# Kernel tuning notes

Hardware: AMD Instinct MI355X
Metric: run time of the kernel (lower is better)

## Reference

```python
import jax, jax.numpy as jnp
import numpy as np

ALPHA = 0.4
MAX_STEPS = 10
GATE_WARMUP = 1.0

def _l2n(x):  # F.normalize(dim=-1), eps=1e-12
    return x / jnp.maximum(jnp.linalg.norm(x, axis=-1, keepdims=True), 1e-12)

def _ln(x, g, b):  # nn.LayerNorm, eps=1e-5
    m = jnp.mean(x, -1, keepdims=True)
    v = jnp.mean((x - m) ** 2, -1, keepdims=True)
    return (x - m) * jax.lax.rsqrt(v + 1e-5) * g + b

def _gelu(x):  # torch F.gelu default = exact erf
    return jax.nn.gelu(x, approximate=False)

def setup_inputs() -> dict:
    key = jax.random.key(0)
    ks = jax.random.split(key, 12)
    B, T, V, D, H = 4, 256, 50257, 768, 3072
    f32 = jnp.float32
    s = lambda k, shape, sc: jax.random.normal(k, shape, dtype=f32) * sc
    return {
        'token_ids': jax.random.randint(ks[0], (B, T), 0, V),
        'embedding': s(ks[1], (V, D), 0.02),      # nn.Embedding table
        'V0': s(ks[2], (D, H), 0.02), 'b0': jnp.zeros((H,), f32),  # hierarchy layer 0
        'V1': s(ks[3], (H, D), 0.02), 'b1': jnp.zeros((D,), f32),  # hierarchy layer 1
        'W1': s(ks[4], (D, D), 0.005), 'c1': jnp.zeros((D,), f32), # core_proj[0]
        'W2': s(ks[5], (D, D), 0.005), 'c2': jnp.zeros((D,), f32), # core_proj[2]
        'Wg': s(ks[6], (2 * D, D), 0.005), 'bg': jnp.zeros((D,), f32),  # gate_proj
        'Wt': s(ks[7], (D, D), 0.01),              # temporal_proj (no bias)
        'gamma': jnp.ones((D,), f32), 'beta': jnp.zeros((D,), f32),    # out_norm
        'Wl': s(ks[8], (D, V), 0.02),              # lm_head (no bias)
        'R_weight': s(ks[9], (D, D), 0.01),        # buffer (orthogonal-ish, small)
    }

def reference(token_ids, embedding, V0, b0, V1, b1, W1, c1, W2, c2, Wg, bg, Wt, gamma, beta, Wl, R_weight):
    B = token_ids.shape[0]
    D = embedding.shape[1]

    def step(carry, idx):
        h_prev, x2 = carry  # h_prev: [B,D] recurrent state; x2: settled hierarchy state [B,D]
        emb = _l2n(embedding[idx])                       # [B,D]
        h_prev_d = jax.lax.stop_gradient(h_prev)         # .detach()
        temporal_raw = h_prev_d @ R_weight               # [B,D]
        ctx = emb + ALPHA * temporal_raw
        # hierarchy.infer_and_learn under no_grad: iterative relaxation toward the
        # feedforward settled state over max_steps iterations.
        ctx_d = jax.lax.stop_gradient(ctx)
        target = _gelu(_gelu(ctx_d @ V0 + b0) @ V1 + b1)
        x2 = jax.lax.fori_loop(0, MAX_STEPS, lambda i, x: 0.5 * x + 0.5 * target, x2)
        x2 = jax.lax.stop_gradient(x2)
        core_settled = _l2n(x2)
        # differentiable shadow path through V0/b0/V1/b1
        core_shadow = _l2n(_gelu(_gelu(ctx @ V0 + b0) @ V1 + b1))
        core_blended = 0.5 * core_shadow + 0.5 * core_settled
        core_feat = _gelu(core_blended @ W1 + c1) @ W2 + c2      # core_proj MLP
        temporal_feat = temporal_raw @ Wt
        gate = jax.nn.sigmoid(jnp.concatenate([emb, core_feat], axis=-1) @ Wg + bg)
        g = gate * GATE_WARMUP
        h_t = g * (core_feat + ALPHA * temporal_feat) + (1.0 - g) * emb
        h_t = _ln(h_t, gamma, beta)
        logits = h_t @ Wl                                # [B,V]
        return (jax.lax.stop_gradient(h_t), x2), logits

    init = (jnp.zeros((B, D), embedding.dtype), jnp.zeros((B, D), embedding.dtype))
    _, logits = jax.lax.scan(step, init, token_ids.T)    # [T,B,V]
    return jnp.transpose(logits, (1, 0, 2))              # [B,T,V]
```

## Files before the change

### kernel.cpp

```cpp
#include <hip/hip_runtime.h>


typedef __attribute__((ext_vector_type(8))) short short8;
typedef __attribute__((ext_vector_type(4))) float f32x4;
typedef unsigned long long u64;

__device__ __forceinline__ unsigned short f2b(float f){
  unsigned int u = __builtin_bit_cast(unsigned int, f);
  u += 0x7fffu + ((u >> 16) & 1u);
  return (unsigned short)(u >> 16);
}
__device__ __forceinline__ float b2f(unsigned short v){
  return __builtin_bit_cast(float, ((unsigned int)v) << 16);
}
__device__ __forceinline__ float geluf(float x){
  return 0.5f * x * (1.0f + erff(x * 0.70710678118654752440f));
}
__device__ __forceinline__ float wsum(float v){
  #pragma unroll
  for (int o = 32; o; o >>= 1) v += __shfl_xor(v, o, 64);
  return v;
}
__device__ __forceinline__ u64 pk3t(float a, float b, float c, unsigned tag){
  return (u64)f2b(a) | ((u64)f2b(b) << 16) | ((u64)f2b(c) << 32) | ((u64)(tag & 0xffffu) << 48);
}
__device__ __forceinline__ void st64(u64* p, u64 v){
  __hip_atomic_store(p, v, __ATOMIC_RELAXED, __HIP_MEMORY_SCOPE_AGENT);
}
__device__ __forceinline__ void stflag(int* p, int v){
  __hip_atomic_store(p, v, __ATOMIC_RELAXED, __HIP_MEMORY_SCOPE_AGENT);
}
__device__ __forceinline__ int ldflag(const int* p){
  return __hip_atomic_load(p, __ATOMIC_RELAXED, __HIP_MEMORY_SCOPE_AGENT);
}
__device__ __forceinline__ void vm0(){ asm volatile("s_waitcnt vmcnt(0)" ::: "memory"); }

#define F0(ph,g) (((ph)*256 + (g))*16)
#define F1(ph,a) (16384 + ((ph)*16 + (a))*16)

__global__ __launch_bounds__(256) void transpose_f2b(
    const float* __restrict__ src, unsigned short* __restrict__ dst,
    int N, int rowoff)
{
  __shared__ unsigned short tile[32][33];
  const int nb = blockIdx.x * 32, kb = blockIdx.y * 32;
  const int tx = threadIdx.x & 31, ty = threadIdx.x >> 5;
  #pragma unroll
  for (int i = 0; i < 4; ++i) {
    int k = kb + ty + 8*i, n = nb + tx;
    unsigned short v = 0;
    if (n < N) v = f2b(src[(size_t)(rowoff + k)*N + n]);
    tile[ty + 8*i][tx] = v;
  }
  __syncthreads();
  #pragma unroll
  for (int i = 0; i < 4; ++i) {
    int n = nb + ty + 8*i;
    if (n < N) dst[(size_t)n*768 + kb + tx] = tile[tx][ty + 8*i];
  }
}

__global__ __launch_bounds__(256) void embed_kernel(
    const int* __restrict__ tok, const float* __restrict__ emb,
    float* __restrict__ emb_all)
{
  const int row = blockIdx.x, tid = threadIdx.x;
  const int id = tok[row];
  const float* e = emb + (size_t)id * 768;
  float v0 = e[tid], v1 = e[tid+256], v2 = e[tid+512];
  float ssq = wsum(v0*v0 + v1*v1 + v2*v2);
  __shared__ float red[4];
  if ((tid & 63) == 0) red[tid >> 6] = ssq;
  __syncthreads();
  float inv = 1.0f / fmaxf(sqrtf(red[0]+red[1]+red[2]+red[3]), 1e-12f);
  float* o = emb_all + (size_t)row * 768;
  o[tid] = v0*inv; o[tid+256] = v1*inv; o[tid+512] = v2*inv;
}

__global__ void gbias_kernel(const float* __restrict__ c2,
                             const float* __restrict__ Wg,
                             float* __restrict__ gbias)
{
  int c = blockIdx.x * 256 + threadIdx.x;
  if (c >= 768) return;
  float s = 0.f;
  for (int k = 0; k < 768; ++k) s += c2[k] * Wg[(size_t)(768 + k)*768 + c];
  gbias[c] = s;
}

template<int BMODE>
__global__ __launch_bounds__(256) void gemm_kernel(
    const float* __restrict__ A, const void* __restrict__ Bp,
    float* __restrict__ C, const float* __restrict__ bias,
    int M, int N, int q, int r)
{
  const int x = blockIdx.x;
  const int s = blockIdx.y;
  const int mtiles = M >> 6;
  const int cnt_x = q + (x < r ? 1 : 0);
  if (s >= cnt_x * mtiles) return;
  const int off_x = x*q + (x < r ? x : r);
  const int nt = off_x + s / mtiles;
  const int mt = s % mtiles;
  const int m0 = mt << 6, n0 = nt << 6;
  const int w = threadIdx.x >> 6, l = threadIdx.x & 63;
  const int lrow = l & 15, lk8 = (l >> 4) << 3;
  const int arow = m0 + w*16 + lrow;
  f32x4 acc[4] = {f32x4{0,0,0,0}, f32x4{0,0,0,0}, f32x4{0,0,0,0}, f32x4{0,0,0,0}};
  const unsigned short* BT = (const unsigned short*)Bp;
  const float* Bf = (const float*)Bp;

  for (int kk = 0; kk < 768; kk += 32) {
    const float4* ap = (const float4*)(A + (size_t)arow*768 + kk + lk8);
    float4 a0 = ap[0], a1 = ap[1];
    short8 af;
    af[0]=(short)f2b(a0.x); af[1]=(short)f2b(a0.y); af[2]=(short)f2b(a0.z); af[3]=(short)f2b(a0.w);
    af[4]=(short)f2b(a1.x); af[5]=(short)f2b(a1.y); af[6]=(short)f2b(a1.z); af[7]=(short)f2b(a1.w);
    #pragma unroll
    for (int ss = 0; ss < 4; ++ss) {
      const int col = n0 + ss*16 + lrow;
      short8 bf;
      if (BMODE == 0) {
        if (col < N) {
          uint4 raw = *(const uint4*)(BT + (size_t)col*768 + kk + lk8);
          bf = __builtin_bit_cast(short8, raw);
        } else {
          bf = short8{0,0,0,0,0,0,0,0};
        }
      } else {
        #pragma unroll
        for (int j = 0; j < 8; ++j) {
          float v = (col < N) ? Bf[(size_t)(kk + lk8 + j)*N + col] : 0.f;
          bf[j] = (short)f2b(v);
        }
      }
      acc[ss] = __builtin_amdgcn_mfma_f32_16x16x32_bf16(af, bf, acc[ss], 0, 0, 0);
    }
  }
  const int rbase = m0 + w*16 + ((l >> 4) << 2);
  #pragma unroll
  for (int ss = 0; ss < 4; ++ss) {
    const int col = n0 + ss*16 + lrow;
    if (col < N) {
      const float badd = bias ? bias[col] : 0.f;
      #pragma unroll
      for (int rr = 0; rr < 4; ++rr)
        C[(size_t)(rbase + rr)*N + col] = acc[ss][rr] + badd;
    }
  }
}

__global__ __launch_bounds__(256) void recur_kernel(
    const float* __restrict__ RV0, const float* __restrict__ RWt,
    const float* __restrict__ W1,  const float* __restrict__ W2,
    const float* __restrict__ W2G, const float* __restrict__ V1,
    const float* __restrict__ embV0, const float* __restrict__ embWg,
    const float* __restrict__ gbias, const float* __restrict__ emb_all,
    const float* __restrict__ b1, const float* __restrict__ c1,
    const float* __restrict__ c2, const float* __restrict__ gam,
    const float* __restrict__ bet, float* __restrict__ h_all,
    u64* __restrict__ a1_if, u64* __restrict__ tg_if,
    u64* __restrict__ u_if,  u64* __restrict__ pre_if,
    int* __restrict__ flg)
{
  __shared__ float sRV0[12*768];
  __shared__ float sV1[3*3072];
  __shared__ float sW1[3*768];
  __shared__ float sW2[3*768];
  __shared__ float sW2G[3*768];
  __shared__ float sRWt[3*768];
  __shared__ float sX[4*768];
  __shared__ float sX2[4*768];
  __shared__ unsigned short sA1[4*3072];
  __shared__ float sRed[240];
  __shared__ float sTf[16];
  __shared__ float sCst[12];
  __shared__ float sEV0[48];
  __shared__ float sEWg[12];
  __shared__ float sEmb[12];

  const int g = blockIdx.x, tid = threadIdx.x;
  const int wv = tid >> 6, lane = tid & 63;
  const bool isAgg = (g < 16);

  for (int i = tid; i < 12*768; i += 256) {
    int k = i / 12, c = i - k*12;
    sRV0[c*768 + k] = RV0[(size_t)k*3072 + g*12 + c];
  }
  for (int i = tid; i < 3*3072; i += 256) {
    int k = i / 3, c = i - k*3;
    sV1[c*3072 + k] = V1[(size_t)k*768 + g*3 + c];
  }
  for (int i = tid; i < 3*768; i += 256) {
    int k = i / 3, c = i - k*3;
    const int gc = g*3 + c;
    sW1[c*768 + k]  = W1[(size_t)k*768 + gc];
    sW2[c*768 + k]  = W2[(size_t)k*768 + gc];
    sW2G[c*768 + k] = W2G[(size_t)k*768 + gc];
    sRWt[c*768 + k] = RWt[(size_t)k*768 + gc];
  }
  for (int i = tid; i < 4*768; i += 256) sX2[i] = 0.f;
  if (tid < 3)       sCst[tid]     = b1[g*3 + tid];
  else if (tid < 6)  sCst[tid]     = c1[g*3 + tid - 3];
  else if (tid < 9)  sCst[tid]     = c2[g*3 + tid - 6];
  else if (tid < 12) sCst[tid]     = gbias[g*3 + tid - 9];
  const int k0 = lane*12;
  float gamv[12], betv[12];
  #pragma unroll
  for (int i = 0; i < 12; ++i) { gamv[i] = gam[k0+i]; betv[i] = bet[k0+i]; }
  __syncthreads();

  for (int t = 0; t <= 256; ++t) {
    if (t < 256) {
      if (tid >= 64 && tid < 112) {
        const int j = tid - 64, bb = j & 3, c = j >> 2;
        sEV0[c*4 + bb] = embV0[(size_t)(bb*256 + t)*3072 + g*12 + c];
      } else if (tid >= 128 && tid < 140) {
        const int j = tid - 128, bb = j & 3, c = j >> 2;
        sEWg[c*4 + bb] = embWg[(size_t)(bb*256 + t)*768 + g*3 + c];
      } else if (tid >= 140 && tid < 152) {
        const int j = tid - 140, bb = j & 3, c = j >> 2;
        sEmb[c*4 + bb] = emb_all[(size_t)(bb*256 + t)*768 + g*3 + c];
      }
    }

    if (t == 0) {
      for (int i = tid; i < 4*768; i += 256) sX[i] = 0.f;
    } else {
      float4 e0, e1, e2;
      {
        const float4* q4 = (const float4*)(emb_all + (size_t)(wv*256 + t - 1)*768 + lane*12);
        e0 = q4[0]; e1 = q4[1]; e2 = q4[2];
      }
      (void)e0; (void)e1; (void)e2;
      if (isAgg) {
        if (tid < 16)
          while (ldflag(flg + F0(3, g*16 + tid)) < t) __builtin_amdgcn_s_sleep(2);
        __syncthreads();
        if (tid == 0) stflag(flg + F1(3, g), t);
      }
      if (tid < 16)
        while (ldflag(flg + F1(3, tid)) < t) __builtin_amdgcn_s_sleep(8);
      __syncthreads();
      const u64* pm = pre_if + (size_t)(t-1)*1024 + lane*16 + wv;
      u64 w4[4];
      #pragma unroll
      for (int qq = 0; qq < 4; ++qq) w4[qq] = pm[qq*4];
      float pre[12];
      #pragma unroll
      for (int qq = 0; qq < 4; ++qq) {
        pre[qq*3+0] = b2f((unsigned short)(w4[qq]));
        pre[qq*3+1] = b2f((unsigned short)(w4[qq] >> 16));
        pre[qq*3+2] = b2f((unsigned short)(w4[qq] >> 32));
      }
      float s1 = 0.f;
      #pragma unroll
      for (int i = 0; i < 12; ++i) s1 += pre[i];
      s1 = wsum(s1);
      const float mean = s1 * (1.0f/768.0f);
      float s2 = 0.f;
      #pragma unroll
      for (int i = 0; i < 12; ++i) { const float d = pre[i] - mean; s2 += d*d; }
      s2 = wsum(s2);
      const float rstd = 1.0f / sqrtf(s2*(1.0f/768.0f) + 1e-5f);
      float hv[12];
      #pragma unroll
      for (int i = 0; i < 12; ++i) {
        hv[i] = (pre[i] - mean)*rstd*gamv[i] + betv[i];
        sX[wv*768 + k0 + i] = hv[i];
      }
      if (g == 0) {
        float* hp = h_all + (size_t)(wv*256 + t - 1)*768 + k0;
        #pragma unroll
        for (int i = 0; i < 12; ++i) hp[i] = hv[i];
      }
    }
    __syncthreads();
    if (t == 256) break;
    const unsigned tagp = (unsigned)(t + 1);
    const int want = t + 1;

    {
      const int cg = tid >> 6, ks = tid & 63;
      float acc[4][4] = {};
      for (int i = 0; i < 12; ++i) {
        const int k = ks + 64*i;
        const float x0 = sX[k], x1 = sX[768+k], x2v = sX[1536+k], x3 = sX[2304+k];
        #pragma unroll
        for (int j = 0; j < 4; ++j) {
          float w;
          if (cg < 3) w = sRV0[(cg*4 + j)*768 + k];
          else        w = (j < 3) ? sRWt[j*768 + k] : 0.f;
          acc[j][0] += w*x0; acc[j][1] += w*x1; acc[j][2] += w*x2v; acc[j][3] += w*x3;
        }
      }
      #pragma unroll
      for (int j = 0; j < 4; ++j)
        #pragma unroll
        for (int bb = 0; bb < 4; ++bb) {
          const float v = wsum(acc[j][bb]);
          if (lane == 0) sRed[cg*16 + j*4 + bb] = v;
        }
      __syncthreads();
      if (tid < 16) {
        const int bb = tid & 3, w = tid >> 2;
        float v[3];
        #pragma unroll
        for (int s = 0; s < 3; ++s) {
          const int c = w*3 + s;
          const float raw = sRed[(c >> 2)*16 + (c & 3)*4 + bb];
          v[s] = geluf(sEV0[c*4 + bb] + 0.4f*raw);
        }
        st64(a1_if + (size_t)t*4096 + bb*1024 + g*4 + w, pk3t(v[0], v[1], v[2], tagp));
      } else if (tid < 20) {
        const int bb = tid - 16;
        sTf[bb]     = sRed[48 + bb];
        sTf[4 + bb] = sRed[52 + bb];
        sTf[8 + bb] = sRed[56 + bb];
      }
      vm0();
      __syncthreads();
      if (tid == 0) stflag(flg + F0(0, g), want);
    }

    {
      if (isAgg) {
        if (tid < 16)
          while (ldflag(flg + F0(0, g*16 + tid)) < want) __builtin_amdgcn_s_sleep(2);
        __syncthreads();
        if (tid == 0) stflag(flg + F1(0, g), want);
      }
      if (tid < 16)
        while (ldflag(flg + F1(0, tid)) < want) __builtin_amdgcn_s_sleep(8);
      __syncthreads();
      const u64* basep = a1_if + (size_t)t*4096;
      u64 x[16];
      #pragma unroll
      for (int i = 0; i < 16; ++i) x[i] = basep[i*256 + tid];
      #pragma unroll
      for (int i = 0; i < 16; ++i) {
        const int widx = i*256 + tid;
        const int bb = widx >> 10, j = widx & 1023;
        sA1[bb*3072 + 3*j + 0] = (unsigned short)(x[i]);
        sA1[bb*3072 + 3*j + 1] = (unsigned short)(x[i] >> 16);
        sA1[bb*3072 + 3*j + 2] = (unsigned short)(x[i] >> 32);
      }
      __syncthreads();
      const int ks = lane, isub = wv;
      float acc[3][4] = {};
      for (int ip = 0; ip < 12; ++ip) {
        const int k = ks + 64*(isub + 4*ip);
        float xv[4];
        #pragma unroll
        for (int bb = 0; bb < 4; ++bb) xv[bb] = b2f(sA1[bb*3072 + k]);
        #pragma unroll
        for (int c = 0; c < 3; ++c) {
          const float w = sV1[c*3072 + k];
          acc[c][0] += w*xv[0]; acc[c][1] += w*xv[1]; acc[c][2] += w*xv[2]; acc[c][3] += w*xv[3];
        }
      }
      #pragma unroll
      for (int c = 0; c < 3; ++c)
        #pragma unroll
        for (int bb = 0; bb < 4; ++bb) {
          const float v = wsum(acc[c][bb]);
          if (lane == 0) sRed[isub*12 + c*4 + bb] = v;
        }
      __syncthreads();
      if (tid < 4) {
        const int bb = tid;
        float v[3];
        #pragma unroll
        for (int c = 0; c < 3; ++c) {
          float s = sRed[c*4+bb] + sRed[12 + c*4+bb] + sRed[24 + c*4+bb] + sRed[36 + c*4+bb];
          v[c] = geluf(s + sCst[c]);
        }
        st64(tg_if + (size_t)t*1024 + g*4 + bb, pk3t(v[0], v[1], v[2], tagp));
      }
      vm0();
      __syncthreads();
      if (tid == 0) stflag(flg + F0(1, g), want);
    }

    {
      if (isAgg) {
        if (tid < 16)
          while (ldflag(flg + F0(1, g*16 + tid)) < want) __builtin_amdgcn_s_sleep(2);
        __syncthreads();
        if (tid == 0) stflag(flg + F1(1, g), want);
      }
      if (tid < 16)
        while (ldflag(flg + F1(1, tid)) < want) __builtin_amdgcn_s_sleep(8);
      __syncthreads();
      const u64* pm = tg_if + (size_t)t*1024 + lane*16 + wv;
      u64 w4[4];
      #pragma unroll
      for (int qq = 0; qq < 4; ++qq) w4[qq] = pm[qq*4];
      float tv[12];
      #pragma unroll
      for (int qq = 0; qq < 4; ++qq) {
        tv[qq*3+0] = b2f((unsigned short)(w4[qq]));
        tv[qq*3+1] = b2f((unsigned short)(w4[qq] >> 16));
        tv[qq*3+2] = b2f((unsigned short)(w4[qq] >> 32));
      }
      const int xb = wv*768 + lane*12;
      float xv2[12];
      float ssqT = 0.f, ssqX = 0.f;
      #pragma unroll
      for (int i = 0; i < 12; ++i) {
        float xx = sX2[xb + i];
        const float tt = tv[i];
        #pragma unroll
        for (int rr = 0; rr < 10; ++rr) xx = 0.5f*xx + 0.5f*tt;
        sX2[xb + i] = xx; xv2[i] = xx;
        ssqT += tt*tt; ssqX += xx*xx;
      }
      ssqT = wsum(ssqT); ssqX = wsum(ssqX);
      const float invT = 1.0f / fmaxf(sqrtf(ssqT), 1e-12f);
      const float invX = 1.0f / fmaxf(sqrtf(ssqX), 1e-12f);
      #pragma unroll
      for (int i = 0; i < 12; ++i) sX[xb + i] = 0.5f*(tv[i]*invT + xv2[i]*invX);
      __syncthreads();
      const int ks = lane, isub = wv;
      float acc[3][4] = {};
      #pragma unroll
      for (int ip = 0; ip < 3; ++ip) {
        const int k = ks + 64*(isub + 4*ip);
        float xv[4];
        #pragma unroll
        for (int bb = 0; bb < 4; ++bb) xv[bb] = sX[bb*768 + k];
        #pragma unroll
        for (int c = 0; c < 3; ++c) {
          const float w = sW1[c*768 + k];
          acc[c][0] += w*xv[0]; acc[c][1] += w*xv[1]; acc[c][2] += w*xv[2]; acc[c][3] += w*xv[3];
        }
      }
      #pragma unroll
      for (int c = 0; c < 3; ++c)
        #pragma unroll
        for (int bb = 0; bb < 4; ++bb) {
          const float v = wsum(acc[c][bb]);
          if (lane == 0) sRed[isub*12 + c*4 + bb] = v;
        }
      __syncthreads();
      if (tid < 4) {
        const int bb = tid;
        float v[3];
        #pragma unroll
        for (int c = 0; c < 3; ++c) {
          float s = sRed[c*4+bb] + sRed[12 + c*4+bb] + sRed[24 + c*4+bb] + sRed[36 + c*4+bb];
          v[c] = geluf(s + sCst[3 + c]);
        }
        st64(u_if + (size_t)t*1024 + g*4 + bb, pk3t(v[0], v[1], v[2], tagp));
      }
      vm0();
      __syncthreads();
      if (tid == 0) stflag(flg + F0(2, g), want);
    }

    {
      if (isAgg) {
        if (tid < 16)
          while (ldflag(flg + F0(2, g*16 + tid)) < want) __builtin_amdgcn_s_sleep(2);
        __syncthreads();
        if (tid == 0) stflag(flg + F1(2, g), want);
      }
      if (tid < 16)
        while (ldflag(flg + F1(2, tid)) < want) __builtin_amdgcn_s_sleep(8);
      __syncthreads();
      const u64* pm = u_if + (size_t)t*1024 + lane*16 + wv;
      u64 w4[4];
      #pragma unroll
      for (int qq = 0; qq < 4; ++qq) w4[qq] = pm[qq*4];
      const int xb = wv*768 + lane*12;
      #pragma unroll
      for (int qq = 0; qq < 4; ++qq) {
        sX[xb + qq*3 + 0] = b2f((unsigned short)(w4[qq]));
        sX[xb + qq*3 + 1] = b2f((unsigned short)(w4[qq] >> 16));
        sX[xb + qq*3 + 2] = b2f((unsigned short)(w4[qq] >> 32));
      }
      __syncthreads();
      const int ks = lane, isub = wv;
      float acc[6][4] = {};
      #pragma unroll
      for (int ip = 0; ip < 3; ++ip) {
        const int k = ks + 64*(isub + 4*ip);
        float xv[4];
        #pragma unroll
        for (int bb = 0; bb < 4; ++bb) xv[bb] = sX[bb*768 + k];
        #pragma unroll
        for (int c = 0; c < 6; ++c) {
          const float w = (c < 3) ? sW2[c*768 + k] : sW2G[(c-3)*768 + k];
          acc[c][0] += w*xv[0]; acc[c][1] += w*xv[1]; acc[c][2] += w*xv[2]; acc[c][3] += w*xv[3];
        }
      }
      #pragma unroll
      for (int c = 0; c < 6; ++c)
        #pragma unroll
        for (int bb = 0; bb < 4; ++bb) {
          const float v = wsum(acc[c][bb]);
          if (lane == 0) sRed[isub*24 + c*4 + bb] = v;
        }
      __syncthreads();
      if (tid < 4) {
        const int bb = tid;
        float pre3[3];
        #pragma unroll
        for (int c = 0; c < 3; ++c) {
          float sc = sRed[c*4+bb] + sRed[24 + c*4+bb] + sRed[48 + c*4+bb] + sRed[72 + c*4+bb];
          const float cf = sc + sCst[6 + c];
          const int cc = c + 3;
          float sg = sRed[cc*4+bb] + sRed[24 + cc*4+bb] + sRed[48 + cc*4+bb] + sRed[72 + cc*4+bb];
          const float gv = sg + sEWg[c*4 + bb] + sCst[9 + c];
          const float gg = 1.0f / (1.0f + expf(-gv));
          const float em = sEmb[c*4 + bb];
          pre3[c] = gg*(cf + 0.4f*sTf[c*4 + bb]) + (1.0f - gg)*em;
        }
        st64(pre_if + (size_t)t*1024 + g*4 + bb, pk3t(pre3[0], pre3[1], pre3[2], tagp));
      }
      vm0();
      __syncthreads();
      if (tid == 0) stflag(flg + F0(3, g), want);
    }
  }
}

static void launch_gemm(const float* A, const void* B, float* C, const float* bias,
                        int M, int N, int bmode, hipStream_t st)
{
  const int ntiles = (N + 63) / 64;
  const int q = ntiles / 8, r = ntiles % 8;
  const int mtiles = M / 64;
  const int smax = (q + (r ? 1 : 0)) * mtiles;
  dim3 grid(8, smax);
  if (bmode == 0) gemm_kernel<0><<<grid, 256, 0, st>>>(A, B, C, bias, M, N, q, r);
  else            gemm_kernel<1><<<grid, 256, 0, st>>>(A, B, C, bias, M, N, q, r);
}

extern "C" void kernel_launch(void* const* d_in, const int* in_sizes, int n_in,
                              void* d_out, int out_size, void* d_ws, size_t ws_size,
                              hipStream_t stream)
{
  const int*   tok   = (const int*)d_in[0];
  const float* emb   = (const float*)d_in[1];
  const float* V0    = (const float*)d_in[2];
  const float* b0    = (const float*)d_in[3];
  const float* V1    = (const float*)d_in[4];
  const float* b1    = (const float*)d_in[5];
  const float* W1    = (const float*)d_in[6];
  const float* c1    = (const float*)d_in[7];
  const float* W2    = (const float*)d_in[8];
  const float* c2    = (const float*)d_in[9];
  const float* Wg    = (const float*)d_in[10];
  const float* bg    = (const float*)d_in[11];
  const float* Wt    = (const float*)d_in[12];
  const float* gamma = (const float*)d_in[13];
  const float* beta  = (const float*)d_in[14];
  const float* Wl    = (const float*)d_in[15];
  const float* Rw    = (const float*)d_in[16];

  float* outf = (float*)d_out;
  float* emb_all = outf + 0;
  float* RV0     = outf + 786432;
  float* RWt     = outf + 3145728;
  float* W2G     = outf + 3735552;
  float* embV0   = outf + 4325376;
  float* embWg   = outf + 7471104;
  float* gbias   = outf + 8257536;
  unsigned short* V0T  = (unsigned short*)(outf + 8258560);
  unsigned short* WtT  = (unsigned short*)(outf + 9438208);
  unsigned short* WgTT = (unsigned short*)(outf + 9733120);
  unsigned short* WgBT = (unsigned short*)(outf + 10028032);
  u64* a1_if  = (u64*)(outf + 10322944);
  u64* tg_if  = (u64*)(outf + 12428288);
  u64* u_if   = (u64*)(outf + 12954624);
  u64* pre_if = (u64*)(outf + 13480960);
  int* flg    = (int*)(outf + 14007296);

  float* h_all = (float*)d_ws;
  unsigned short* WlT = (unsigned short*)((char*)d_ws + 786432*4);
  const bool bigws = ws_size >= (size_t)(786432*4) + (size_t)38597376*2 + 256;

  hipMemsetAsync(flg, 0, 17408 * sizeof(int), stream);

  transpose_f2b<<<dim3(96, 24),   256, 0, stream>>>(V0, V0T, 3072, 0);
  transpose_f2b<<<dim3(24, 24),   256, 0, stream>>>(Wt, WtT, 768, 0);
  transpose_f2b<<<dim3(24, 24),   256, 0, stream>>>(Wg, WgTT, 768, 0);
  transpose_f2b<<<dim3(24, 24),   256, 0, stream>>>(Wg, WgBT, 768, 768);
  if (bigws)
    transpose_f2b<<<dim3(1572, 24), 256, 0, stream>>>(Wl, WlT, 50257, 0);

  embed_kernel<<<1024, 256, 0, stream>>>(tok, emb, emb_all);
  gbias_kernel<<<3, 256, 0, stream>>>(c2, Wg, gbias);

  launch_gemm(Rw,      V0T,  RV0,   nullptr, 768,  3072, 0, stream);
  launch_gemm(Rw,      WtT,  RWt,   nullptr, 768,  768,  0, stream);
  launch_gemm(W2,      WgBT, W2G,   nullptr, 768,  768,  0, stream);
  launch_gemm(emb_all, V0T,  embV0, b0,      1024, 3072, 0, stream);
  launch_gemm(emb_all, WgTT, embWg, bg,      1024, 768,  0, stream);

  recur_kernel<<<256, 256, 0, stream>>>(
      RV0, RWt, W1, W2, W2G, V1, embV0, embWg, gbias, emb_all,
      b1, c1, c2, gamma, beta, h_all,
      a1_if, tg_if, u_if, pre_if, flg);

  if (bigws) launch_gemm(h_all, WlT, outf, nullptr, 1024, 50257, 0, stream);
  else       launch_gemm(h_all, Wl,  outf, nullptr, 1024, 50257, 1, stream);
}
```

Before: 8.768 ms.

## Replace per-block completion flags with tagged data polling in recurrence sync

Aggregator blocks now poll the 16-bit tag packed into each data word (a1/tg/u/pre interchange buffers) instead of waiting on per-producer flags. This removes the vmcnt(0) drain, the extra barrier and the flag store after each phase, cutting one level of the two-level barrier. It also drops an unused embedding prefetch and collapses the 10-step relaxation into a closed form (multiply by 2^-10). The cost is more polling threads and loads per phase, and correctness now depends on the 64-bit stores being atomic and the tags never aliasing.

```diff
diff --git a/kernel.cpp b/kernel.cpp
--- a/kernel.cpp
+++ b/kernel.cpp
@@ -27,16 +27,20 @@
 __device__ __forceinline__ void st64(u64* p, u64 v){
   __hip_atomic_store(p, v, __ATOMIC_RELAXED, __HIP_MEMORY_SCOPE_AGENT);
 }
+__device__ __forceinline__ u64 ld64(const u64* p){
+  return __hip_atomic_load(p, __ATOMIC_RELAXED, __HIP_MEMORY_SCOPE_AGENT);
+}
 __device__ __forceinline__ void stflag(int* p, int v){
   __hip_atomic_store(p, v, __ATOMIC_RELAXED, __HIP_MEMORY_SCOPE_AGENT);
 }
 __device__ __forceinline__ int ldflag(const int* p){
   return __hip_atomic_load(p, __ATOMIC_RELAXED, __HIP_MEMORY_SCOPE_AGENT);
 }
-__device__ __forceinline__ void vm0(){ asm volatile("s_waitcnt vmcnt(0)" ::: "memory"); }
-
-#define F0(ph,g) (((ph)*256 + (g))*16)
-#define F1(ph,a) (16384 + ((ph)*16 + (a))*16)
+__device__ __forceinline__ void waittag(const u64* p, unsigned want){
+  while ((unsigned)(ld64(p) >> 48) != (want & 0xffffu)) __builtin_amdgcn_s_sleep(2);
+}
+
+#define F1(ph,a) ((((ph)*16) + (a))*16)
 
 __global__ __launch_bounds__(256) void transpose_f2b(
     const float* __restrict__ src, unsigned short* __restrict__ dst,
@@ -227,15 +231,10 @@
     if (t == 0) {
       for (int i = tid; i < 4*768; i += 256) sX[i] = 0.f;
     } else {
-      float4 e0, e1, e2;
-      {
-        const float4* q4 = (const float4*)(emb_all + (size_t)(wv*256 + t - 1)*768 + lane*12);
-        e0 = q4[0]; e1 = q4[1]; e2 = q4[2];
-      }
-      (void)e0; (void)e1; (void)e2;
       if (isAgg) {
-        if (tid < 16)
-          while (ldflag(flg + F0(3, g*16 + tid)) < t) __builtin_amdgcn_s_sleep(2);
+        if (tid < 64)
+          waittag(pre_if + (size_t)(t-1)*1024 + (g*16 + (tid >> 2))*4 + (tid & 3),
+                  (unsigned)t);
         __syncthreads();
         if (tid == 0) stflag(flg + F1(3, g), t);
       }
@@ -318,15 +317,12 @@
         sTf[4 + bb] = sRed[52 + bb];
         sTf[8 + bb] = sRed[56 + bb];
       }
-      vm0();
-      __syncthreads();
-      if (tid == 0) stflag(flg + F0(0, g), want);
     }
 
     {
       if (isAgg) {
-        if (tid < 16)
-          while (ldflag(flg + F0(0, g*16 + tid)) < want) __builtin_amdgcn_s_sleep(2);
+        waittag(a1_if + (size_t)t*4096 + ((tid & 15) >> 2)*1024
+                      + (g*16 + (tid >> 4))*4 + (tid & 3), tagp);
         __syncthreads();
         if (tid == 0) stflag(flg + F1(0, g), want);
       }
@@ -377,15 +373,12 @@
         }
         st64(tg_if + (size_t)t*1024 + g*4 + bb, pk3t(v[0], v[1], v[2], tagp));
       }
-      vm0();
-      __syncthreads();
-      if (tid == 0) stflag(flg + F0(1, g), want);
     }
 
     {
       if (isAgg) {
-        if (tid < 16)
-          while (ldflag(flg + F0(1, g*16 + tid)) < want) __builtin_amdgcn_s_sleep(2);
+        if (tid < 64)
+          waittag(tg_if + (size_t)t*1024 + (g*16 + (tid >> 2))*4 + (tid & 3), tagp);
         __syncthreads();
         if (tid == 0) stflag(flg + F1(1, g), want);
       }
@@ -408,10 +401,8 @@
       float ssqT = 0.f, ssqX = 0.f;
       #pragma unroll
       for (int i = 0; i < 12; ++i) {
-        float xx = sX2[xb + i];
         const float tt = tv[i];
-        #pragma unroll
-        for (int rr = 0; rr < 10; ++rr) xx = 0.5f*xx + 0.5f*tt;
+        const float xx = tt + (sX2[xb + i] - tt) * 0.0009765625f;
         sX2[xb + i] = xx; xv2[i] = xx;
         ssqT += tt*tt; ssqX += xx*xx;
       }
@@ -453,15 +444,12 @@
         }
         st64(u_if + (size_t)t*1024 + g*4 + bb, pk3t(v[0], v[1], v[2], tagp));
       }
-      vm0();
-      __syncthreads();
-      if (tid == 0) stflag(flg + F0(2, g), want);
     }
 
     {
       if (isAgg) {
-        if (tid < 16)
-          while (ldflag(flg + F0(2, g*16 + tid)) < want) __builtin_amdgcn_s_sleep(2);
+        if (tid < 64)
+          waittag(u_if + (size_t)t*1024 + (g*16 + (tid >> 2))*4 + (tid & 3), tagp);
         __syncthreads();
         if (tid == 0) stflag(flg + F1(2, g), want);
       }
@@ -518,9 +506,7 @@
         }
         st64(pre_if + (size_t)t*1024 + g*4 + bb, pk3t(pre3[0], pre3[1], pre3[2], tagp));
       }
-      vm0();
-      __syncthreads();
-      if (tid == 0) stflag(flg + F0(3, g), want);
+      __syncthreads();
     }
   }
 }
@@ -581,7 +567,7 @@
   unsigned short* WlT = (unsigned short*)((char*)d_ws + 786432*4);
   const bool bigws = ws_size >= (size_t)(786432*4) + (size_t)38597376*2 + 256;
 
-  hipMemsetAsync(flg, 0, 17408 * sizeof(int), stream);
+  hipMemsetAsync(flg, 0, 1024 * sizeof(int), stream);
 
   transpose_f2b<<<dim3(96, 24),   256, 0, stream>>>(V0, V0T, 3072, 0);
   transpose_f2b<<<dim3(24, 24),   256, 0, stream>>>(Wt, WtT, 768, 0);
```

Result: faster. 8.392 ms (-4.3%).
